# Kernel tuning notes

Hardware: AMD Instinct MI355X
Metric: run time of the kernel (lower is better)

Reference implementation:

```python
import jax, jax.numpy as jnp
import numpy as np
from jax import lax

LENGTH, WIDTH = 64, 64
INPUT_DIM = 1


def _convlstm_layer(x_tbchw, W, b):
    """Run one ConvLSTM layer over time. x_tbchw: (L,B,Cin,H,W).
    W: (4*hid, Cin+hid, 3, 3), b: (4*hid,). Returns (outputs (L,B,hid,H,W), last_h)."""
    L, B, _, H, Wd = x_tbchw.shape
    hid = W.shape[0] // 4
    h0 = jnp.zeros((B, hid, H, Wd), dtype=x_tbchw.dtype)
    c0 = jnp.zeros((B, hid, H, Wd), dtype=x_tbchw.dtype)

    def step(carry, xt):
        h, c = carry
        z = lax.conv_general_dilated(
            jnp.concatenate([xt, h], axis=1), W,
            window_strides=(1, 1), padding='SAME',
            dimension_numbers=('NCHW', 'OIHW', 'NCHW'))
        z = z + b[None, :, None, None]
        cc_i, cc_f, cc_o, cc_g = jnp.split(z, 4, axis=1)
        c_next = jax.nn.sigmoid(cc_f) * c + jax.nn.sigmoid(cc_i) * jnp.tanh(cc_g)
        h_next = jax.nn.sigmoid(cc_o) * jnp.tanh(c_next)
        return (h_next, c_next), h_next

    (h_last, _), outs = lax.scan(step, (h0, c0), x_tbchw)
    return outs, h_last


def setup_inputs() -> dict:
    key = jax.random.key(0)
    k1, k2, k3 = jax.random.split(key, 3)
    B, L, N = 16, 12, LENGTH * WIDTH
    emd, out_len = 128, 12
    return {
        'history_data': jax.random.normal(k1, (B, L, N, 1), dtype=jnp.float32),
        'future_data': jnp.zeros((B, L, N, 1), dtype=jnp.float32),
        'W0': jax.random.normal(k2, (4 * emd, INPUT_DIM + emd, 3, 3), dtype=jnp.float32) * 0.05,
        'b0': jnp.zeros((4 * emd,), dtype=jnp.float32),
        'W1': jax.random.normal(k3, (4 * out_len, emd + out_len, 3, 3), dtype=jnp.float32) * 0.05,
        'b1': jnp.zeros((4 * out_len,), dtype=jnp.float32),
        'batch_seen': 0,
        'epoch': 0,
        'train': 1,
    }


def reference(history_data, future_data, W0, b0, W1, b1, batch_seen, epoch, train):
    B, L, N, C = history_data.shape
    # (B,L,1,H,W) -> (L,B,1,H,W) for time-major scan
    x = history_data[..., :INPUT_DIM].reshape(B, L, INPUT_DIM, LENGTH, WIDTH)
    x = jnp.transpose(x, (1, 0, 2, 3, 4))
    outs0, _ = _convlstm_layer(x, W0, b0)          # (L,B,emd,H,W)
    _, h_last = _convlstm_layer(outs0, W1, b1)     # (B,out_len,H,W)
    prediction = h_last.reshape(B, L, LENGTH * WIDTH)[..., None]  # (B,L,N,1)
    return prediction
```

## Files before the change

### kernel.cpp

```cpp
#include <hip/hip_runtime.h>
#include <hip/hip_bf16.h>


typedef __attribute__((ext_vector_type(8))) short short8;
typedef __attribute__((ext_vector_type(4))) float float4v;

#define CS 160
#define KT0 1152
#define KTOT 1440
#define RSTR 2112
#define BSTR4 8448
#define BSTR6 12672

__device__ __forceinline__ float sigf(float x) { return 1.f / (1.f + __expf(-x)); }
__device__ __forceinline__ short f2hs(float v) {
  _Float16 h = (_Float16)v;
  return *(short*)&h;
}
__device__ __forceinline__ float bs2f(short s) {
  __hip_bfloat16 h; *(short*)&h = s; return __bfloat162float(h);
}
__device__ __forceinline__ short f2bs(float v) {
  __hip_bfloat16 h = __float2bfloat16(v);
  return *(short*)&h;
}

__device__ __forceinline__ void async_ld16(const short* g, short* l) {
  __builtin_amdgcn_global_load_lds(
      (const __attribute__((address_space(1))) unsigned int*)g,
      (__attribute__((address_space(3))) unsigned int*)l, 16, 0, 0);
}

__device__ __forceinline__ void stage_one4(const short* __restrict__ rowPtr, bool rowOK,
                                           short* dstRow, int lane,
                                           const short* __restrict__ zp, int j) {
  int e = j * 64 + lane;
  int px = e >> 2, v = e & 3;
  int xx = px - 1;
  bool ok = rowOK && (xx >= 0);
  const short* g = ok ? (rowPtr + (size_t)xx * CS + v * 8) : zp;
  async_ld16(g, dstRow + e * 8);
}

__device__ __forceinline__ void stage_row4(const short* __restrict__ rowPtr, bool rowOK,
                                           short* dstRow, int lane,
                                           const short* __restrict__ zp) {
  #pragma unroll
  for (int j = 0; j < 4; ++j) stage_one4(rowPtr, rowOK, dstRow, lane, zp, j);
}

__device__ __forceinline__ short8 tail_load(const short* __restrict__ srcChunk,
                                            bool rowOK, int lane) {
  short8 tv = {0, 0, 0, 0, 0, 0, 0, 0};
  if (lane < 4 && rowOK) tv = *(const short8*)(srcChunk + (size_t)63 * CS + lane * 8);
  return tv;
}

__device__ __forceinline__ void tail_write(short* dstRow, int lane, short8 tv) {
  if (lane < 8) {
    short8 w = {0, 0, 0, 0, 0, 0, 0, 0};
    if (lane < 4) w = tv;
    *(short8*)(dstRow + (64 + (lane >> 2)) * 32 + (lane & 3) * 8) = w;
  }
}

__global__ void detect_dtype(const unsigned short* __restrict__ w0, int* __restrict__ flag) {
  int lane = threadIdx.x;
  int cnt = 0;
  for (int i = 0; i < 4; ++i) {
    unsigned short u = w0[2 * (lane + 64 * i)];
    int e = (u >> 7) & 0xFF;
    unsigned long long b = __ballot(e >= 0xC0);
    cnt += __popcll(b);
  }
  if (lane == 0) *flag = (cnt > 32) ? 1 : 0;
}

__global__ void canon_b(const void* __restrict__ b0, const void* __restrict__ b1,
                        float* __restrict__ Bc0, float* __restrict__ Bc1,
                        const int* __restrict__ flag) {
  int i = blockIdx.x * 256 + threadIdx.x;
  int fl = *flag;
  if (i < 512) {
    float v = fl ? ((const float*)b0)[i] : bs2f(((const short*)b0)[i]);
    if (!isfinite(v) || fabsf(v) > 1e4f) v = 0.f;
    Bc0[i] = v;
  } else if (i < 560) {
    int j = i - 512;
    float v = fl ? ((const float*)b1)[j] : bs2f(((const short*)b1)[j]);
    if (!isfinite(v) || fabsf(v) > 1e4f) v = 0.f;
    Bc1[j] = v;
  }
}

__device__ __forceinline__ float ldw(const void* W, int idx, int fl) {
  float w = fl ? ((const float*)W)[idx] : bs2f(((const short*)W)[idx]);
  if (!isfinite(w) || fabsf(w) > 1e4f) w = 0.f;
  return w;
}

__global__ void prep_w0(const void* __restrict__ W0, short* __restrict__ Wp,
                        const int* __restrict__ flag) {
  int i = blockIdx.x * 256 + threadIdx.x;
  if (i >= 512 * KT0) return;
  int fl = *flag;
  int co = i / KT0, k = i - co * KT0;
  int tap = k >> 7, c = k & 127;
  Wp[i] = f2hs(ldw(W0, (co * 129 + 1 + c) * 9 + tap, fl));
}

__global__ void prep_wx(const void* __restrict__ W0, short* __restrict__ Wx,
                        const int* __restrict__ flag) {
  int i = blockIdx.x * 256 + threadIdx.x;
  if (i >= 512 * 16) return;
  int fl = *flag;
  int co = i >> 4, k = i & 15;
  float w = (k < 9) ? ldw(W0, (co * 129) * 9 + k, fl) : 0.f;
  Wx[i] = f2hs(w);
}

__global__ void prep_w1(const void* __restrict__ W1, short* __restrict__ Wp,
                        const int* __restrict__ flag) {
  int i = blockIdx.x * 256 + threadIdx.x;
  if (i >= 48 * KTOT) return;
  int fl = *flag;
  int co = i / KTOT, k = i - co * KTOT;
  int tap = k / CS, c = k - tap * CS;
  float w = (c < 140) ? ldw(W1, (co * 140 + c) * 9 + tap, fl) : 0.f;
  Wp[i] = f2hs(w);
}

__global__ void prep_xtap(const void* __restrict__ hist, short* __restrict__ Xtap,
                          const int* __restrict__ flag) {
  int i = blockIdx.x * 256 + threadIdx.x;
  int t = i >> 16, p = i & 65535;
  int b = p >> 12, pix = p & 4095, y = pix >> 6, x = pix & 63;
  int fl = *flag;
  short8 lo = {0, 0, 0, 0, 0, 0, 0, 0}, hi = {0, 0, 0, 0, 0, 0, 0, 0};
  #pragma unroll
  for (int k = 0; k < 9; ++k) {
    int dy = k / 3, dx = k - dy * 3;
    int yy = y + dy - 1, xx = x + dx - 1;
    float f = 0.f;
    if (yy >= 0 && yy < 64 && xx >= 0 && xx < 64) {
      int hidx = (b * 12 + t) * 4096 + yy * 64 + xx;
      f = fl ? ((const float*)hist)[hidx] : bs2f(((const short*)hist)[hidx]);
      if (!isfinite(f) || fabsf(f) > 1e4f) f = 0.f;
    }
    if (k < 8) lo[k] = f2hs(f); else hi[k - 8] = f2hs(f);
  }
  *(short8*)(Xtap + (size_t)i * 16) = lo;
  *(short8*)(Xtap + (size_t)i * 16 + 8) = hi;
}

__global__ __launch_bounds__(256, 2) void gemm_gate0(
    const short* __restrict__ Pcur, short* __restrict__ Pnext,
    const short* __restrict__ Wp, const short* __restrict__ Wx,
    const float* __restrict__ Bc0, float* __restrict__ C0,
    const short* __restrict__ Xtap, const short* __restrict__ zp, int t) {
  int pbx = blockIdx.x;
  int xcd = pbx & 7, i = pbx >> 3;
  int mt = xcd * 32 + (i & 31);
  int nt = i >> 5;
  int b = mt >> 4, y0 = (mt & 15) * 4;
  int tid = threadIdx.x, wave = tid >> 6, lane = tid & 63;
  int ln15 = lane & 15, quad = lane >> 4;
  int wm = wave & 1, wn = wave >> 1;
  int hc = nt * 32 + wn * 16 + ln15;

  __shared__ __align__(16) short halo[2 * BSTR6];

  float4v acc[8][4];
  #pragma unroll
  for (int i2 = 0; i2 < 8; ++i2)
    #pragma unroll
    for (int j = 0; j < 4; ++j) acc[i2][j] = (float4v){0.f, 0.f, 0.f, 0.f};

  const short* wbase = Wp + (size_t)hc * KT0 + quad * 8;
  short8 bcur[4], bnxt[4];
  #pragma unroll
  for (int g = 0; g < 4; ++g)
    bcur[g] = *(const short8*)(wbase + (size_t)g * 128 * KT0);

  int yyA = y0 - 1 + wave;
  bool okA = (yyA >= 0) && (yyA < 64);
  const short* baseA = Pcur + (size_t)((b * 64 + yyA) * 64) * CS;
  int yyB = y0 + 3 + wave;
  bool okB = (wave < 2) && (yyB < 64);
  const short* baseB = Pcur + (size_t)((b * 64 + yyB) * 64) * CS;

  bool hiQ = quad >= 2;
  short8 ax[8], bxr[4];
  #pragma unroll
  for (int mf = 0; mf < 8; ++mf) {
    int row = y0 + wm * 2 + (mf >> 2);
    int pixB = (b * 64 + row) * 64 + (mf & 3) * 16 + ln15;
    ax[mf] = *(const short8*)(Xtap + ((size_t)t * 65536 + pixB) * 16 + (quad & 1) * 8);
  }
  #pragma unroll
  for (int g = 0; g < 4; ++g) {
    const short* wxp = Wx + (size_t)(g * 128 + hc) * 16 + (quad & 1) * 8;
    bxr[g] = *(const short8*)(hiQ ? zp : wxp);
  }
  short8 tA = tail_load(baseA, okA, lane);
  short8 tB = tail_load(baseB, okB, lane);

  stage_row4(baseA, okA, halo + wave * RSTR, lane, zp);
  if (wave < 2) stage_row4(baseB, okB, halo + (4 + wave) * RSTR, lane, zp);

  #pragma unroll
  for (int g = 0; g < 4; ++g)
    #pragma unroll
    for (int mf = 0; mf < 8; ++mf)
      acc[mf][g] = __builtin_amdgcn_mfma_f32_16x16x32_f16(ax[mf], bxr[g], acc[mf][g], 0, 0, 0);

  tail_write(halo + wave * RSTR, lane, tA);
  if (wave < 2) tail_write(halo + (4 + wave) * RSTR, lane, tB);
  __syncthreads();

  for (int ch = 0; ch < 4; ++ch) {
    int c0 = ch * 32;
    const short* cur = halo + (ch & 1) * BSTR6;
    short* nd = halo + ((ch + 1) & 1) * BSTR6;
    const short* srcA = baseA + c0 + 32;
    const short* srcB = baseB + c0 + 32;
    short8 nA = {0, 0, 0, 0, 0, 0, 0, 0}, nB = {0, 0, 0, 0, 0, 0, 0, 0};
    if (ch < 3) {
      nA = tail_load(srcA, okA, lane);
      if (wave < 2) nB = tail_load(srcB, okB, lane);
    }
    #pragma unroll
    for (int tap = 0; tap < 9; ++tap) {
      int dy = tap / 3, dx = tap - dy * 3;
      if (ch < 3 && tap < 4) {
        stage_one4(srcA, okA, nd + wave * RSTR, lane, zp, tap);
        if (wave < 2) stage_one4(srcB, okB, nd + (4 + wave) * RSTR, lane, zp, tap);
      }
      int ntap = (tap < 8) ? tap + 1 : 0;
      int nc0 = (tap < 8) ? c0 : ((ch < 3) ? c0 + 32 : c0);
      #pragma unroll
      for (int g = 0; g < 4; ++g)
        bnxt[g] = *(const short8*)(wbase + (size_t)g * 128 * KT0 + ntap * 128 + nc0);

      short8 af[8];
      #pragma unroll
      for (int mf = 0; mf < 8; ++mf)
        af[mf] = *(const short8*)&cur[(wm * 2 + (mf >> 2) + dy) * RSTR
                                      + ((mf & 3) * 16 + ln15 + dx) * 32 + quad * 8];
      #pragma unroll
      for (int g = 0; g < 4; ++g)
        #pragma unroll
        for (int mf = 0; mf < 8; ++mf)
          acc[mf][g] = __builtin_amdgcn_mfma_f32_16x16x32_f16(af[mf], bcur[g], acc[mf][g], 0, 0, 0);
      #pragma unroll
      for (int g = 0; g < 4; ++g) bcur[g] = bnxt[g];
    }
    if (ch < 3) {
      tail_write(nd + wave * RSTR, lane, nA);
      if (wave < 2) tail_write(nd + (4 + wave) * RSTR, lane, nB);
    }
    __syncthreads();
  }

  float bi = Bc0[hc], bff = Bc0[128 + hc], bo = Bc0[256 + hc], bg = Bc0[384 + hc];
  #pragma unroll
  for (int mf = 0; mf < 8; ++mf) {
    int row = y0 + wm * 2 + (mf >> 2);
    int pixRow = (b * 64 + row) * 64;
    #pragma unroll
    for (int r = 0; r < 4; ++r) {
      int x = (mf & 3) * 16 + quad * 4 + r;
      int pix = pixRow + x;
      float zi = acc[mf][0][r] + bi;
      float zf = acc[mf][1][r] + bff;
      float zo = acc[mf][2][r] + bo;
      float zg = acc[mf][3][r] + bg;
      float cprev = C0[(size_t)pix * 128 + hc];
      float cn = sigf(zf) * cprev + sigf(zi) * tanhf(zg);
      float hn = sigf(zo) * tanhf(cn);
      C0[(size_t)pix * 128 + hc] = cn;
      Pnext[(size_t)pix * CS + hc] = f2hs(hn);
    }
  }
}

__global__ __launch_bounds__(256, 2) void gemm_gate1(
    const short* __restrict__ Prd, short* __restrict__ Pwr,
    const short* __restrict__ Wp, const float* __restrict__ Bc1,
    float* __restrict__ C1, void* __restrict__ outp,
    const short* __restrict__ zp, const int* __restrict__ flagp, int t) {
  int pbx = blockIdx.x;
  int bid = (pbx & 7) * 64 + (pbx >> 3);
  int b = bid >> 5, y0 = (bid & 31) * 2;
  int tid = threadIdx.x, wave = tid >> 6, lane = tid & 63;
  int ln15 = lane & 15, quad = lane >> 4;
  int w = wave & 1, kp = wave >> 1;
  int flagv = *flagp;

  __shared__ __align__(16) short halo[2 * BSTR4];

  float4v acc[4][3];
  #pragma unroll
  for (int i = 0; i < 4; ++i)
    #pragma unroll
    for (int j = 0; j < 3; ++j) acc[i][j] = (float4v){0.f, 0.f, 0.f, 0.f};

  int yy = y0 - 1 + wave;
  bool rowOK = (yy >= 0) && (yy < 64);
  const short* rowBase = Prd + (size_t)((b * 64 + yy) * 64) * CS;

  const short* wbase = Wp + (size_t)ln15 * KTOT + quad * 8;
  short8 bcur[3];
  #pragma unroll
  for (int nf = 0; nf < 3; ++nf)
    bcur[nf] = *(const short8*)(wbase + (size_t)nf * 16 * KTOT + kp * CS);

  short8 tP = tail_load(rowBase, rowOK, lane);
  stage_row4(rowBase, rowOK, halo + wave * RSTR, lane, zp);
  tail_write(halo + wave * RSTR, lane, tP);
  __syncthreads();

  for (int ch = 0; ch < 5; ++ch) {
    int c0 = ch * 32;
    const short* cur = halo + (ch & 1) * BSTR4;
    short* nxtDst = halo + ((ch + 1) & 1) * BSTR4 + wave * RSTR;
    const short* nxtSrc = rowBase + c0 + 32;
    short8 nP = {0, 0, 0, 0, 0, 0, 0, 0};
    if (ch < 4) nP = tail_load(nxtSrc, rowOK, lane);
    int ts = (kp + ch * 9) & 1;
    #pragma unroll
    for (int tt = 0; tt < 5; ++tt) {
      int tap = ts + tt * 2;
      if (tap <= 8) {
        int dy = tap / 3, dx = tap - dy * 3;
        if (ch < 4 && tt < 4)
          stage_one4(nxtSrc, rowOK, nxtDst, lane, zp, tt);
        int ntap = tap + 2, nc0 = c0;
        if (ntap > 8) { ntap -= 9; nc0 = (ch < 4) ? c0 + 32 : c0; }
        short8 bnxt[3];
        #pragma unroll
        for (int nf = 0; nf < 3; ++nf)
          bnxt[nf] = *(const short8*)(wbase + (size_t)nf * 16 * KTOT + ntap * CS + nc0);

        short8 af[4];
        #pragma unroll
        for (int mf = 0; mf < 4; ++mf)
          af[mf] = *(const short8*)&cur[(w + dy) * RSTR + (mf * 16 + ln15 + dx) * 32
                                        + quad * 8];
        #pragma unroll
        for (int nf = 0; nf < 3; ++nf)
          #pragma unroll
          for (int mf = 0; mf < 4; ++mf)
            acc[mf][nf] = __builtin_amdgcn_mfma_f32_16x16x32_f16(af[mf], bcur[nf], acc[mf][nf], 0, 0, 0);
        #pragma unroll
        for (int nf = 0; nf < 3; ++nf) bcur[nf] = bnxt[nf];
      }
    }
    if (ch < 4) tail_write(nxtDst, lane, nP);
    __syncthreads();
  }

  float* zbuf = (float*)halo;
  if (kp == 0) {
    #pragma unroll
    for (int mf = 0; mf < 4; ++mf)
      #pragma unroll
      for (int nf = 0; nf < 3; ++nf)
        #pragma unroll
        for (int r = 0; r < 4; ++r) {
          int pxl = w * 64 + mf * 16 + quad * 4 + r;
          zbuf[pxl * 48 + nf * 16 + ln15] = acc[mf][nf][r];
        }
  }
  __syncthreads();
  if (kp == 1) {
    #pragma unroll
    for (int mf = 0; mf < 4; ++mf)
      #pragma unroll
      for (int nf = 0; nf < 3; ++nf)
        #pragma unroll
        for (int r = 0; r < 4; ++r) {
          int pxl = w * 64 + mf * 16 + quad * 4 + r;
          zbuf[pxl * 48 + nf * 16 + ln15] += acc[mf][nf][r];
        }
  }
  __syncthreads();

  #pragma unroll
  for (int k = 0; k < 6; ++k) {
    int id = k * 256 + tid;
    int hc = id >> 7, pxl = id & 127;
    float zi = zbuf[pxl * 48 + hc]      + Bc1[hc];
    float zf = zbuf[pxl * 48 + 12 + hc] + Bc1[12 + hc];
    float zo = zbuf[pxl * 48 + 24 + hc] + Bc1[24 + hc];
    float zg = zbuf[pxl * 48 + 36 + hc] + Bc1[36 + hc];
    int y = y0 + (pxl >> 6), x = pxl & 63;
    int pix = (b * 64 + y) * 64 + x;
    float cprev = C1[(size_t)pix * 12 + hc];
    float cn = sigf(zf) * cprev + sigf(zi) * tanhf(zg);
    float hn = sigf(zo) * tanhf(cn);
    C1[(size_t)pix * 12 + hc] = cn;
    Pwr[(size_t)pix * CS + 128 + hc] = f2hs(hn);
    if (t == 11) {
      int oidx = (b * 12 + hc) * 4096 + y * 64 + x;
      if (flagv) ((float*)outp)[oidx] = hn;
      else ((short*)outp)[oidx] = f2bs(hn);
    }
  }
}

extern "C" void kernel_launch(void* const* d_in, const int* in_sizes, int n_in,
                              void* d_out, int out_size, void* d_ws, size_t ws_size,
                              hipStream_t stream) {
  const void* hist = d_in[0];
  const void* W0 = d_in[2];
  const void* b0 = d_in[3];
  const void* W1 = d_in[4];
  const void* b1 = d_in[5];

  char* ws = (char*)d_ws;
  const size_t PszB = (size_t)16 * 4096 * CS * 2;
  short* P[2] = {(short*)ws, (short*)(ws + PszB)};
  float* C0 = (float*)(ws + 2 * PszB);
  const size_t C0e = 2 * PszB + 33554432;
  float* C1 = (float*)(ws + C0e);
  const size_t C1e = C0e + 3145728;
  short* zp = (short*)(ws + C1e);
  const size_t zpe = C1e + 256;
  short* Xtap = (short*)(ws + zpe);
  const size_t Xte = zpe + (size_t)12 * 65536 * 16 * 2;
  short* Wp0 = (short*)(ws + Xte);
  const size_t W0e = Xte + (size_t)512 * KT0 * 2;
  short* Wx0 = (short*)(ws + W0e);
  const size_t Wxe = W0e + 512 * 16 * 2;
  short* Wp1 = (short*)(ws + Wxe);
  const size_t W1e = Wxe + (size_t)48 * KTOT * 2;
  float* Bc0 = (float*)(ws + W1e);
  float* Bc1 = (float*)(ws + W1e + 2048);
  int* flag = (int*)(ws + W1e + 2048 + 192);

  hipMemsetAsync(ws, 0, zpe, stream);
  detect_dtype<<<1, 64, 0, stream>>>((const unsigned short*)W0, flag);
  canon_b<<<3, 256, 0, stream>>>(b0, b1, Bc0, Bc1, flag);
  prep_w0<<<(512 * KT0 + 255) / 256, 256, 0, stream>>>(W0, Wp0, flag);
  prep_wx<<<32, 256, 0, stream>>>(W0, Wx0, flag);
  prep_w1<<<(48 * KTOT + 255) / 256, 256, 0, stream>>>(W1, Wp1, flag);
  prep_xtap<<<3072, 256, 0, stream>>>(hist, Xtap, flag);

  for (int t = 0; t < 12; ++t) {
    gemm_gate0<<<1024, 256, 0, stream>>>(P[t & 1], P[(t + 1) & 1], Wp0, Wx0, Bc0, C0,
                                         Xtap, zp, t);
    gemm_gate1<<<512, 256, 0, stream>>>(P[(t + 1) & 1], P[t & 1], Wp1, Bc1, C1,
                                        d_out, zp, flag, t);
  }
}
```

Baseline: 1.814 ms.

## Fuse layer-0 step k and layer-1 step k-1 into one skewed launch

The two per-timestep GEMM+gate kernels become device functions and are called from a single fused kernel. Each launch k runs layer-0 timestep k and layer-1 timestep k-1, with blocks split 2:1 across the grid. Layer-1 now writes its hidden state into the next ping-pong buffer instead of the one it reads. This cuts the launch count from 24 to 13 and lets the smaller layer-1 work fill the tail of the layer-0 grid. In exchange, layer-1 blocks now reserve the larger layer-0 shared-memory allocation, and the whole recurrence depends on the more complex skewed schedule being correct.

```diff
diff --git a/kernel.cpp b/kernel.cpp
--- a/kernel.cpp
+++ b/kernel.cpp
@@ -153,22 +153,19 @@
   *(short8*)(Xtap + (size_t)i * 16 + 8) = hi;
 }
 
-__global__ __launch_bounds__(256, 2) void gemm_gate0(
+__device__ __forceinline__ void gg0_body(
+    int xcd, int j0, short* halo,
     const short* __restrict__ Pcur, short* __restrict__ Pnext,
     const short* __restrict__ Wp, const short* __restrict__ Wx,
     const float* __restrict__ Bc0, float* __restrict__ C0,
     const short* __restrict__ Xtap, const short* __restrict__ zp, int t) {
-  int pbx = blockIdx.x;
-  int xcd = pbx & 7, i = pbx >> 3;
-  int mt = xcd * 32 + (i & 31);
-  int nt = i >> 5;
+  int mt = xcd * 32 + (j0 & 31);
+  int nt = j0 >> 5;
   int b = mt >> 4, y0 = (mt & 15) * 4;
   int tid = threadIdx.x, wave = tid >> 6, lane = tid & 63;
   int ln15 = lane & 15, quad = lane >> 4;
   int wm = wave & 1, wn = wave >> 1;
   int hc = nt * 32 + wn * 16 + ln15;
-
-  __shared__ __align__(16) short halo[2 * BSTR6];
 
   float4v acc[8][4];
   #pragma unroll
@@ -284,20 +281,17 @@
   }
 }
 
-__global__ __launch_bounds__(256, 2) void gemm_gate1(
+__device__ __forceinline__ void gg1_body(
+    int xcd, int j1, short* halo,
     const short* __restrict__ Prd, short* __restrict__ Pwr,
     const short* __restrict__ Wp, const float* __restrict__ Bc1,
     float* __restrict__ C1, void* __restrict__ outp,
-    const short* __restrict__ zp, const int* __restrict__ flagp, int t) {
-  int pbx = blockIdx.x;
-  int bid = (pbx & 7) * 64 + (pbx >> 3);
+    const short* __restrict__ zp, int flagv, int t) {
+  int bid = xcd * 64 + j1;
   int b = bid >> 5, y0 = (bid & 31) * 2;
   int tid = threadIdx.x, wave = tid >> 6, lane = tid & 63;
   int ln15 = lane & 15, quad = lane >> 4;
   int w = wave & 1, kp = wave >> 1;
-  int flagv = *flagp;
-
-  __shared__ __align__(16) short halo[2 * BSTR4];
 
   float4v acc[4][3];
   #pragma unroll
@@ -405,6 +399,30 @@
       int oidx = (b * 12 + hc) * 4096 + y * 64 + x;
       if (flagv) ((float*)outp)[oidx] = hn;
       else ((short*)outp)[oidx] = f2bs(hn);
+    }
+  }
+}
+
+__global__ __launch_bounds__(256, 2) void fused_step(
+    const short* __restrict__ Pr, short* __restrict__ Pw,
+    const short* __restrict__ Wp0, const short* __restrict__ Wx,
+    const float* __restrict__ Bc0, float* __restrict__ C0,
+    const short* __restrict__ Xtap,
+    const short* __restrict__ Wp1, const float* __restrict__ Bc1,
+    float* __restrict__ C1, void* __restrict__ outp,
+    const short* __restrict__ zp, const int* __restrict__ flagp, int k) {
+  __shared__ __align__(16) short halo[2 * BSTR6];
+  int bx = blockIdx.x;
+  int xcd = bx & 7, j = bx >> 3;
+  if (j % 3 != 2) {
+    if (k < 12) {
+      int j0 = j - j / 3;
+      gg0_body(xcd, j0, halo, Pr, Pw, Wp0, Wx, Bc0, C0, Xtap, zp, k);
+    }
+  } else {
+    if (k >= 1) {
+      int j1 = j / 3;
+      gg1_body(xcd, j1, halo, Pr, Pw, Wp1, Bc1, C1, outp, zp, *flagp, k - 1);
     }
   }
 }
@@ -447,10 +465,7 @@
   prep_w1<<<(48 * KTOT + 255) / 256, 256, 0, stream>>>(W1, Wp1, flag);
   prep_xtap<<<3072, 256, 0, stream>>>(hist, Xtap, flag);
 
-  for (int t = 0; t < 12; ++t) {
-    gemm_gate0<<<1024, 256, 0, stream>>>(P[t & 1], P[(t + 1) & 1], Wp0, Wx0, Bc0, C0,
-                                         Xtap, zp, t);
-    gemm_gate1<<<512, 256, 0, stream>>>(P[(t + 1) & 1], P[t & 1], Wp1, Bc1, C1,
-                                        d_out, zp, flag, t);
-  }
-}
+  for (int k = 0; k <= 12; ++k)
+    fused_step<<<1536, 256, 0, stream>>>(P[k & 1], P[(k + 1) & 1], Wp0, Wx0, Bc0, C0,
+                                         Xtap, Wp1, Bc1, C1, d_out, zp, flag, k);
+}
```

New measurement: 2.076 ms. 1.14x slower.
